# Kernel tuning notes

Hardware: AMD Instinct MI355X
Metric: run time of the kernel (lower is better)

Reference implementation:

```python
import jax, jax.numpy as jnp
import numpy as np

EPS = 0.05  # mesh.epsilon boundary band


def _pool_one(adj, image, vs, edges):
    # adj: [N,N] bool, image: [N,F] f32, vs: [N,2] f32 in [0,1], edges: [2,E] int32
    N, F = image.shape
    E = edges.shape[1]
    K = N // 2                      # out_target
    tgt_kills = N - K               # number of vertices removed
    v0, v1 = edges[0], edges[1]
    # heap key = sum of squares of concat(image[v0], image[v1])
    cost = jnp.sum(image[v0] * image[v0], -1) + jnp.sum(image[v1] * image[v1], -1)
    def bnd(p):
        return (p[:, 0] < EPS) | (p[:, 0] > 1 - EPS) | (p[:, 1] < EPS) | (p[:, 1] > 1 - EPS)
    ok = ~(bnd(vs[v0]) | bnd(vs[v1]))   # boundary_mask = ~is_boundary
    # heappop of [value, id] lists == stable sort by cost (ties broken by edge id)
    order = jnp.argsort(cost)
    # sequential greedy collapse: kill v1 if edge interior and both endpoints alive
    def step(carry, eid):
        mask, nk = carry
        a, b = v0[eid], v1[eid]
        acc = ok[eid] & mask[a] & mask[b] & (nk < tgt_kills)
        mask = mask.at[b].set(mask[b] & ~acc)
        return (mask, nk + acc.astype(jnp.int32)), acc
    (mask, _), accepts = jax.lax.scan(step, (jnp.ones(N, bool), jnp.int32(0)), order)
    sv0, sv1 = v0[order], v1[order]
    # mapping m: dead vertex -> absorbing vertex (identity elsewhere)
    dead = jnp.where(accepts, sv1, N)          # N = out-of-range -> dropped
    m = jnp.arange(N).at[dead].set(sv0, mode='drop')
    # update_matrix: scatter-add collapsed vertex features into absorber rows
    upd = jnp.zeros_like(image).at[jnp.where(accepts, sv0, N)].add(image[sv1], mode='drop')
    image2 = image + upd
    # merge_vertex on adjacency: union rows then columns of merged vertices
    A = adj.astype(jnp.uint8)
    A1 = jnp.zeros_like(A).at[m].max(A)        # merge rows
    A2 = jnp.zeros_like(A1).at[m].max(A1.T).T  # merge cols
    alive = jnp.nonzero(mask, size=K, fill_value=0)[0]  # exactly K survivors
    adj_out = A2[alive][:, alive].astype(bool) & ~jnp.eye(K, dtype=bool)
    return adj_out, image2[alive]


def setup_inputs() -> dict:
    key = jax.random.key(0)
    k1, k2, k3, k4, k5 = jax.random.split(key, 5)
    B, N, F, E = 4, 8192, 64, 65536
    adj = jax.random.bernoulli(k1, 0.002, (B, N, N))
    image = jax.random.normal(k2, (B, N, F), jnp.float32)
    vs = jax.random.uniform(k3, (B, N, 2), dtype=jnp.float32)
    a = jax.random.randint(k4, (B, 1, E), 0, N)
    off = jax.random.randint(k5, (B, 1, E), 1, N)
    b = (a + off) % N                           # guarantee v0 != v1
    edges = jnp.concatenate([a, b], axis=1).astype(jnp.int32)
    return {"adj": adj, "image": image, "vs": vs, "edges": edges}


def reference(adj, image, vs, edges):
    # returns (pooled adjacency [B,N//2,N//2] bool, pooled features [B,N//2,F])
    return jax.vmap(_pool_one)(adj, image, vs, edges)
```

## Files before the change

kernel.cpp:

```cpp
#include <hip/hip_runtime.h>
#include <stdint.h>

typedef unsigned long long u64;
typedef unsigned int u32;
typedef unsigned char u8;

#define Bn 4
#define Nv 8192
#define Fd 64
#define Ed 65536
#define Kv 4096
#define TGTK 4096
#define NW 256
#define SC 8192

#define SWZ8(i) ((i) ^ (((i) >> 3) & 15))

#define WS_FLAGS   ((size_t)0)
#define WS_ACCCNT  ((size_t)256)
#define WS_OUTBITS ((size_t)512)
#define OUTBITS_BYTES ((size_t)Bn*Kv*128*4)
#define WS_ZERO_BYTES (WS_OUTBITS + OUTBITS_BYTES)
#define WS_KEYS    (WS_ZERO_BYTES)
#define WS_SQ      (WS_KEYS + (size_t)Bn*Ed*8)
#define WS_BND     (WS_SQ + (size_t)Bn*Nv*4)
#define WS_MAP     (WS_BND + (size_t)Bn*Nv)
#define WS_POS     (WS_MAP + (size_t)Bn*Nv*4)
#define WS_PM      (WS_POS + (size_t)Bn*Nv*4)
#define WS_ALIVEW  (WS_PM + (size_t)Bn*Nv*4)
#define WS_ALIST   (WS_ALIVEW + (size_t)Bn*NW*4)
#define WS_ACC     (WS_ALIST + (size_t)Bn*Kv*4)
#define WS_PACK    (WS_ACC + (size_t)Bn*TGTK*2*4)
#define WS_SPACK   (WS_PACK + (size_t)Bn*Ed*4)

__global__ void k_detect(const u8* adj, u32* flags) {
    int tid = blockIdx.x * blockDim.x + threadIdx.x;
    const u32* w = (const u32*)adj;
    bool f0 = false, f1 = false, f2 = false, f3 = false;
    for (int i = tid; i < (1 << 19); i += gridDim.x * blockDim.x) {
        u32 v = w[i];
        f0 |= (v & 0x000000FFu) != 0;
        f1 |= (v & 0x0000FF00u) != 0;
        f2 |= (v & 0x00FF0000u) != 0;
        f3 |= (v & 0xFF000000u) != 0;
    }
    u32 m = 0;
    if (__ballot(f0)) m |= 1;
    if (__ballot(f1)) m |= 2;
    if (__ballot(f2)) m |= 4;
    if (__ballot(f3)) m |= 8;
    if ((threadIdx.x & 63) == 0 && m) atomicOr(flags, m);
}

__global__ void k_vertex(const float* image, const float* vs, float* sq, u8* bnd, int* map) {
#pragma clang fp contract(off)
    int idx = blockIdx.x * 256 + threadIdx.x;
    if (idx >= Bn * Nv) return;
    const float* row = image + (size_t)idx * Fd;
    float r[8];
#pragma unroll
    for (int j = 0; j < 8; ++j) r[j] = row[j] * row[j];
#pragma unroll
    for (int i = 8; i < 64; i += 8)
#pragma unroll
        for (int j = 0; j < 8; ++j) r[j] += row[i + j] * row[i + j];
    float s = ((r[0] + r[1]) + (r[2] + r[3])) + ((r[4] + r[5]) + (r[6] + r[7]));
    sq[idx] = s;
    float x = vs[(size_t)idx * 2], y = vs[(size_t)idx * 2 + 1];
    const float LO = 0.05f;
    const float HI = (float)(1.0 - 0.05);
    bnd[idx] = ((x < LO) || (x > HI) || (y < LO) || (y > HI)) ? 1 : 0;
    map[idx] = idx & (Nv - 1);
}

__global__ void k_edge(const int* edges, const float* sq, const u8* bnd, u64* keys, u32* pack) {
    int idx = blockIdx.x * 256 + threadIdx.x;
    if (idx >= Bn * Ed) return;
    int b = idx >> 16, e = idx & (Ed - 1);
    int v0 = edges[(size_t)b * 2 * Ed + e];
    int v1 = edges[(size_t)b * 2 * Ed + Ed + e];
    float c = sq[b * Nv + v0] + sq[b * Nv + v1];
    u32 okk = (!bnd[b * Nv + v0] && !bnd[b * Nv + v1]) ? 1u : 0u;
    pack[idx] = (u32)v0 | ((u32)v1 << 13) | (okk << 26);
    keys[idx] = okk ? (((u64)__float_as_uint(c) << 16) | (u32)e) : ~0ull;
}

__device__ __forceinline__ void bitonic_cas(u64* s, int i, int pa, bool asc) {
    u64 a = s[i], c = s[pa];
    if ((a > c) == asc) { s[i] = c; s[pa] = a; }
}
__device__ __forceinline__ void cex(u64& a, u64& b, bool asc) {
    if ((a > b) == asc) { u64 t = a; a = b; b = t; }
}

__global__ __launch_bounds__(1024) void k_sortA(u64* keys) {
    __shared__ u64 s[SC];
    int b = blockIdx.x >> 3, ch = blockIdx.x & 7;
    u64* base = keys + (size_t)b * Ed + (size_t)ch * SC;
    int gb = ch * SC;
    int t8 = threadIdx.x * 8;
    u64 r[8];
#pragma unroll
    for (int u = 0; u < 8; ++u) r[u] = base[t8 + u];
    cex(r[0], r[1], true); cex(r[2], r[3], false); cex(r[4], r[5], true); cex(r[6], r[7], false);
    cex(r[0], r[2], true); cex(r[1], r[3], true); cex(r[4], r[6], false); cex(r[5], r[7], false);
    cex(r[0], r[1], true); cex(r[2], r[3], true); cex(r[4], r[5], false); cex(r[6], r[7], false);
    {
        bool a8 = (((gb + t8) & 8) == 0);
        cex(r[0], r[4], a8); cex(r[1], r[5], a8); cex(r[2], r[6], a8); cex(r[3], r[7], a8);
        cex(r[0], r[2], a8); cex(r[1], r[3], a8); cex(r[4], r[6], a8); cex(r[5], r[7], a8);
        cex(r[0], r[1], a8); cex(r[2], r[3], a8); cex(r[4], r[5], a8); cex(r[6], r[7], a8);
    }
#pragma unroll
    for (int u = 0; u < 8; ++u) s[SWZ8(t8 + u)] = r[u];
    __syncthreads();
    for (int k = 16; k <= SC; k <<= 1) {
        for (int j = k >> 1; j >= 8; j >>= 1) {
#pragma unroll
            for (int p = 0; p < SC / 2048; ++p) {
                int t = p * 1024 + threadIdx.x;
                int i = ((t & ~(j - 1)) << 1) | (t & (j - 1));
                bool asc = (((gb + i) & k) == 0);
                bitonic_cas(s, SWZ8(i), SWZ8(i | j), asc);
            }
            __syncthreads();
        }
        bool asc = (((gb + t8) & k) == 0);
#pragma unroll
        for (int u = 0; u < 8; ++u) r[u] = s[SWZ8(t8 + u)];
        cex(r[0], r[4], asc); cex(r[1], r[5], asc); cex(r[2], r[6], asc); cex(r[3], r[7], asc);
        cex(r[0], r[2], asc); cex(r[1], r[3], asc); cex(r[4], r[6], asc); cex(r[5], r[7], asc);
        cex(r[0], r[1], asc); cex(r[2], r[3], asc); cex(r[4], r[5], asc); cex(r[6], r[7], asc);
        if (k == SC) {
#pragma unroll
            for (int u = 0; u < 8; ++u) base[t8 + u] = r[u];
        } else {
#pragma unroll
            for (int u = 0; u < 8; ++u) s[SWZ8(t8 + u)] = r[u];
            __syncthreads();
        }
    }
}

__global__ __launch_bounds__(1024) void k_sortV(u64* keys, int k) {
    int b = blockIdx.x >> 3;
    int c = (blockIdx.x & 7) * 1024 + threadIdx.x;
    u64* base = keys + (size_t)b * Ed + c;
    u64 r[8];
#pragma unroll
    for (int m = 0; m < 8; ++m) r[m] = base[(size_t)m * 8192];
    if (k == 65536) {
        cex(r[0], r[4], true); cex(r[1], r[5], true); cex(r[2], r[6], true); cex(r[3], r[7], true);
        cex(r[0], r[2], true); cex(r[1], r[3], true); cex(r[4], r[6], true); cex(r[5], r[7], true);
        cex(r[0], r[1], true); cex(r[2], r[3], true); cex(r[4], r[5], true); cex(r[6], r[7], true);
    } else if (k == 32768) {
        cex(r[0], r[2], true); cex(r[1], r[3], true); cex(r[4], r[6], false); cex(r[5], r[7], false);
        cex(r[0], r[1], true); cex(r[2], r[3], true); cex(r[4], r[5], false); cex(r[6], r[7], false);
    } else {
        cex(r[0], r[1], true); cex(r[2], r[3], false); cex(r[4], r[5], true); cex(r[6], r[7], false);
    }
#pragma unroll
    for (int m = 0; m < 8; ++m) base[(size_t)m * 8192] = r[m];
}

__global__ __launch_bounds__(1024) void k_sortC(u64* keys, int k,
                                                const u32* pack, u32* spack, int dofin) {
    __shared__ u64 s[SC];
    int b = blockIdx.x >> 3, ch = blockIdx.x & 7;
    u64* base = keys + (size_t)b * Ed + (size_t)ch * SC;
    int gb = ch * SC;
    for (int p = 0; p < SC / 1024; ++p) {
        int i = p * 1024 + threadIdx.x;
        s[SWZ8(i)] = base[i];
    }
    __syncthreads();
    bool asc = ((gb & k) == 0);
    for (int j = SC / 2; j >= 8; j >>= 1) {
#pragma unroll
        for (int p = 0; p < SC / 2048; ++p) {
            int t = p * 1024 + threadIdx.x;
            int i = ((t & ~(j - 1)) << 1) | (t & (j - 1));
            bitonic_cas(s, SWZ8(i), SWZ8(i | j), asc);
        }
        __syncthreads();
    }
    int t8 = threadIdx.x * 8;
    u64 r[8];
#pragma unroll
    for (int u = 0; u < 8; ++u) r[u] = s[SWZ8(t8 + u)];
    cex(r[0], r[4], asc); cex(r[1], r[5], asc); cex(r[2], r[6], asc); cex(r[3], r[7], asc);
    cex(r[0], r[2], asc); cex(r[1], r[3], asc); cex(r[4], r[6], asc); cex(r[5], r[7], asc);
    cex(r[0], r[1], asc); cex(r[2], r[3], asc); cex(r[4], r[5], asc); cex(r[6], r[7], asc);
    if (dofin) {
        const u32* pk = pack + (size_t)b * Ed;
        u32* sp = spack + (size_t)b * Ed + (size_t)ch * SC;
#pragma unroll
        for (int u = 0; u < 8; ++u)
            sp[t8 + u] = (r[u] == ~0ull) ? 0u : pk[(u32)(r[u] & 0xFFFFu)];
    } else {
#pragma unroll
        for (int u = 0; u < 8; ++u) base[t8 + u] = r[u];
    }
}

__global__ __launch_bounds__(64) void k_greedy(const u32* spack, int* map, u32* aliveW,
                                               int* accList, u32* accCnt) {
    int b = blockIdx.x;
    int lane = threadIdx.x;
    __shared__ u32 alive[NW];
    __shared__ u32 mlane[Nv];
    for (int i = lane; i < NW; i += 64) alive[i] = 0xFFFFFFFFu;
    for (int i = lane; i < Nv; i += 64) mlane[i] = 0x7FFFFFFFu;
    const u32* sp = spack + (size_t)b * Ed;
    u32 pa = sp[lane], pb = sp[64 + lane];
    __syncthreads();
    int nk = 0;
    const int G = Ed / 128;
    for (int g = 0; g < G; ++g) {
        u32 na = 0u, nb = 0u;
        if (g + 1 < G) { na = sp[(g + 1) * 128 + lane]; nb = sp[(g + 1) * 128 + 64 + lane]; }
        int v0a = pa & 8191, v1a = (pa >> 13) & 8191; bool oka = (pa >> 26) & 1u;
        int v0b = pb & 8191, v1b = (pb >> 13) & 8191; bool okb = (pb >> 26) & 1u;
        u32 gi = (u32)(G + 1 - g) << 8;
        if (oka) atomicMin(&mlane[v1a], gi | (u32)lane);
        if (okb) atomicMin(&mlane[v1b], gi | (u32)(64 + lane));
        __syncthreads();
        u32 aw0a = alive[v0a >> 5], aw1a = alive[v1a >> 5];
        u32 aw0b = alive[v0b >> 5], aw1b = alive[v1b >> 5];
        u32 m0a = mlane[v0a], m1a = mlane[v1a];
        u32 m0b = mlane[v0b], m1b = mlane[v1b];
        bool specA = oka && ((aw0a >> (v0a & 31)) & 1u) && ((aw1a >> (v1a & 31)) & 1u);
        bool specB = okb && ((aw0b >> (v0b & 31)) & 1u) && ((aw1b >> (v1b & 31)) & 1u);
        u32 slA = (u32)lane, slB = (u32)(64 + lane);
        bool confA = specA && ((((m0a & 0xFFFFFF00u) == gi) && ((m0a & 255u) < slA)) ||
                               (((m1a & 0xFFFFFF00u) == gi) && ((m1a & 255u) < slA)));
        bool confB = specB && ((((m0b & 0xFFFFFF00u) == gi) && ((m0b & 255u) < slB)) ||
                               (((m1b & 0xFFFFFF00u) == gi) && ((m1b & 255u) < slB)));
        u64 specLo = __ballot(specA), specHi = __ballot(specB);
        u64 confLo = __ballot(confA), confHi = __ballot(confB);
        u64 accLo = specLo & ~confLo, accHi = specHi & ~confHi;
        u64 rem = confLo;
        while (rem) {
            int l = __ffsll((unsigned long long)rem) - 1; rem &= rem - 1;
            int bv0 = __shfl(v0a, l), bv1 = __shfl(v1a, l);
            bool kA = ((accLo >> lane) & 1ull) && (lane < l) && (v1a == bv0 || v1a == bv1);
            if (__ballot(kA) == 0ull) accLo |= 1ull << l;
        }
        rem = confHi;
        while (rem) {
            int l = __ffsll((unsigned long long)rem) - 1; rem &= rem - 1;
            int bv0 = __shfl(v0b, l), bv1 = __shfl(v1b, l);
            bool kA = ((accLo >> lane) & 1ull) && (v1a == bv0 || v1a == bv1);
            bool kB = ((accHi >> lane) & 1ull) && (lane < l) && (v1b == bv0 || v1b == bv1);
            if ((__ballot(kA) | __ballot(kB)) == 0ull) accHi |= 1ull << l;
        }
        int cntLo = __popcll(accLo);
        int cnt = cntLo + __popcll(accHi);
        int remK = TGTK - nk;
        bool accA = (accLo >> lane) & 1ull;
        bool accB = (accHi >> lane) & 1ull;
        if (cnt > remK) {
            int rA = __popcll(accLo & ((1ull << lane) - 1ull));
            if (accA && rA >= remK) accA = false;
            int rB = cntLo + __popcll(accHi & ((1ull << lane) - 1ull));
            if (accB && rB >= remK) accB = false;
            accLo = __ballot(accA); accHi = __ballot(accB);
            cntLo = __popcll(accLo);
            cnt = remK;
        }
        if (accA) {
            atomicAnd(&alive[v1a >> 5], ~(1u << (v1a & 31)));
            map[(size_t)b * Nv + v1a] = v0a;
            int r = __popcll(accLo & ((1ull << lane) - 1ull));
            int slot = nk + r;
            accList[((size_t)b * TGTK + slot) * 2] = v0a;
            accList[((size_t)b * TGTK + slot) * 2 + 1] = v1a;
        }
        if (accB) {
            atomicAnd(&alive[v1b >> 5], ~(1u << (v1b & 31)));
            map[(size_t)b * Nv + v1b] = v0b;
            int r = cntLo + __popcll(accHi & ((1ull << lane) - 1ull));
            int slot = nk + r;
            accList[((size_t)b * TGTK + slot) * 2] = v0b;
            accList[((size_t)b * TGTK + slot) * 2 + 1] = v1b;
        }
        nk += cnt;
        if (nk >= TGTK) break;
        pa = na; pb = nb;
    }
    for (int i = lane; i < NW; i += 64) aliveW[b * NW + i] = alive[i];
    if (lane == 0) accCnt[b] = (u32)nk;
}

__global__ __launch_bounds__(256) void k_scan(const u32* aliveW, const int* map,
                                              int* pos, int* pm, int* alist) {
    int b = blockIdx.x, tid = threadIdx.x;
    __shared__ u32 cnt[256];
    __shared__ u32 off[256];
    u32 w = aliveW[b * NW + tid];
    cnt[tid] = __popc(w);
    __syncthreads();
    if (tid == 0) { u32 s = 0; for (int i = 0; i < 256; ++i) { off[i] = s; s += cnt[i]; } }
    __syncthreads();
    u32 base = off[tid];
    int* posb = pos + (size_t)b * Nv;
    int* alb = alist + (size_t)b * Kv;
    for (int bit = 0; bit < 32; ++bit) {
        int v = tid * 32 + bit;
        int p = -1;
        if ((w >> bit) & 1u) {
            if (base < Kv) { p = (int)base; alb[base] = v; }
            base++;
        }
        posb[v] = p;
    }
    __syncthreads();
    const int* mapb = map + (size_t)b * Nv;
    int* pmb = pm + (size_t)b * Nv;
    for (int v = tid; v < Nv; v += 256) pmb[v] = posb[mapb[v]];
}

__global__ void k_fcopy(const float* image, const int* alist, float* outF) {
    int idx = blockIdx.x * 256 + threadIdx.x;
    if (idx >= Bn * Kv * 16) return;
    int b = idx >> 16, r = idx & 65535;
    int x = r >> 4, f4 = r & 15;
    int src = alist[b * Kv + x];
    const float4* s = (const float4*)(image + ((size_t)(b * Nv + src)) * Fd) + f4;
    float4* d = (float4*)(outF + ((size_t)(b * Kv + x)) * Fd) + f4;
    *d = *s;
}

__global__ __launch_bounds__(64) void k_fscat(const float* image, const int* accList,
                                              const u32* accCnt, const int* pos, float* outF) {
    int b = blockIdx.x >> 12, e = blockIdx.x & 4095;
    if (e >= (int)accCnt[b]) return;
    int v0 = accList[((size_t)b * TGTK + e) * 2];
    int v1 = accList[((size_t)b * TGTK + e) * 2 + 1];
    int x = pos[(size_t)b * Nv + v0];
    if (x < 0) return;
    int f = threadIdx.x;
    atomicAdd(outF + ((size_t)(b * Kv + x)) * Fd + f,
              image[((size_t)(b * Nv + v1)) * Fd + f]);
}

__global__ __launch_bounds__(256) void k_merge(const u8* adj, const u32* flags,
                                               const int* pm, u32* outbits) {
    int bi = blockIdx.x;
    int b = bi >> 13, i = bi & (Nv - 1);
    int t = pm[(size_t)b * Nv + i];
    if (t < 0) return;
    __shared__ u32 bits[Kv / 32];
    int tid = threadIdx.x;
    if (tid < 128) bits[tid] = 0;
    __syncthreads();
    const int* pmb = pm + (size_t)b * Nv;
    u32 fw = flags[0];
    bool bytefmt = (fw & 1) && (fw & 8);
    auto put = [&](int col) {
        int c = pmb[col];
        if (c >= 0) atomicOr(&bits[c >> 5], 1u << (c & 31));
    };
    if (bytefmt) {
        const uint4* row = (const uint4*)(adj + ((size_t)b * Nv + i) * Nv);
#pragma unroll
        for (int it = 0; it < 2; ++it) {
            uint4 v = row[it * 256 + tid];
            if (v.x | v.y | v.z | v.w) {
                int cb = (it * 256 + tid) * 16;
                u32 wv[4] = { v.x, v.y, v.z, v.w };
                for (int q = 0; q < 4; ++q) {
                    u32 u = wv[q];
                    if (!u) continue;
#pragma unroll
                    for (int kk = 0; kk < 4; ++kk)
                        if ((u >> (8 * kk)) & 0xFFu) put(cb + q * 4 + kk);
                }
            }
        }
    } else {
        const uint4* row = (const uint4*)((const u32*)adj + ((size_t)b * Nv + i) * Nv);
        for (int it = 0; it < 8; ++it) {
            uint4 v = row[it * 256 + tid];
            int cb = (it * 256 + tid) * 4;
            if (v.x) put(cb);
            if (v.y) put(cb + 1);
            if (v.z) put(cb + 2);
            if (v.w) put(cb + 3);
        }
    }
    __syncthreads();
    if (tid < 128) {
        u32 bw = bits[tid];
        if (bw) atomicOr(&outbits[((size_t)b * Kv + t) * 128 + tid], bw);
    }
}

__global__ void k_expand(const u32* outbits, float* out) {
    int idx = blockIdx.x;
    int tid = threadIdx.x;
    int b = idx >> 14, r = idx & 16383;
    int x = r >> 2, seg = r & 3;
    int c0 = seg * 1024 + tid * 4;
    u32 w = outbits[((size_t)b * Kv + x) * 128 + (c0 >> 5)];
    u32 nib = (w >> (c0 & 31)) & 0xFu;
    float4 f;
    f.x = (nib & 1) ? 1.f : 0.f;
    f.y = (nib & 2) ? 1.f : 0.f;
    f.z = (nib & 4) ? 1.f : 0.f;
    f.w = (nib & 8) ? 1.f : 0.f;
    if (x >= c0 && x < c0 + 4) ((float*)&f)[x - c0] = 0.f;
    *((float4*)(out + ((size_t)(b * Kv + x)) * Kv + c0)) = f;
}

extern "C" void kernel_launch(void* const* d_in, const int* in_sizes, int n_in,
                              void* d_out, int out_size, void* d_ws, size_t ws_size,
                              hipStream_t stream) {
    const u8* adj = (const u8*)d_in[0];
    const float* image = (const float*)d_in[1];
    const float* vs = (const float*)d_in[2];
    const int* edges = (const int*)d_in[3];
    char* ws = (char*)d_ws;
    u32* flags = (u32*)(ws + WS_FLAGS);
    u32* accCnt = (u32*)(ws + WS_ACCCNT);
    u32* outbits = (u32*)(ws + WS_OUTBITS);
    u64* keys = (u64*)(ws + WS_KEYS);
    float* sq = (float*)(ws + WS_SQ);
    u8* bnd = (u8*)(ws + WS_BND);
    int* map = (int*)(ws + WS_MAP);
    int* pos = (int*)(ws + WS_POS);
    int* pm = (int*)(ws + WS_PM);
    u32* aliveW = (u32*)(ws + WS_ALIVEW);
    int* alist = (int*)(ws + WS_ALIST);
    int* accList = (int*)(ws + WS_ACC);
    u32* pack = (u32*)(ws + WS_PACK);
    u32* spack = (u32*)(ws + WS_SPACK);
    float* outA = (float*)d_out;
    float* outF = outA + (size_t)Bn * Kv * Kv;

    hipMemsetAsync(d_ws, 0, WS_ZERO_BYTES, stream);
    k_detect<<<64, 256, 0, stream>>>(adj, flags);
    k_vertex<<<Bn * Nv / 256, 256, 0, stream>>>(image, vs, sq, bnd, map);
    k_edge<<<Bn * Ed / 256, 256, 0, stream>>>(edges, sq, bnd, keys, pack);
    k_sortA<<<Bn * 8, 1024, 0, stream>>>(keys);
    k_sortV<<<Bn * 8, 1024, 0, stream>>>(keys, 16384);
    k_sortC<<<Bn * 8, 1024, 0, stream>>>(keys, 16384, pack, spack, 0);
    k_sortV<<<Bn * 8, 1024, 0, stream>>>(keys, 32768);
    k_sortC<<<Bn * 8, 1024, 0, stream>>>(keys, 32768, pack, spack, 0);
    k_sortV<<<Bn * 8, 1024, 0, stream>>>(keys, 65536);
    k_sortC<<<Bn * 8, 1024, 0, stream>>>(keys, 65536, pack, spack, 1);
    k_greedy<<<Bn, 64, 0, stream>>>(spack, map, aliveW, accList, accCnt);
    k_scan<<<Bn, 256, 0, stream>>>(aliveW, map, pos, pm, alist);
    k_fcopy<<<Bn * Kv * 16 / 256, 256, 0, stream>>>(image, alist, outF);
    k_fscat<<<Bn * TGTK, 64, 0, stream>>>(image, accList, accCnt, pos, outF);
    k_merge<<<Bn * Nv, 256, 0, stream>>>(adj, flags, pm, outbits);
    k_expand<<<Bn * Kv * 4, 256, 0, stream>>>(outbits, outA);
}
```

Before: 1.761 ms.

## Fuse detect into vertex, sort V+C stages, and scan into greedy kernel

Folds the adjacency-format detection into the first 64 blocks of the vertex kernel, and merges each global bitonic cross-chunk step with the following in-shared-memory chunk sort so each block recomputes the needed cross-chunk compare-exchanges while loading. The alive-bitmap prefix scan and position mapping move into the tail of the single-wave greedy kernel, using shuffles and shared memory instead of a separate launch. This removes five kernel launches and a global round trip of the key array per merge stage. In exchange, the fused sort kernel reads 2-8x more key data per block, and the scan now runs on only 64 threads per batch.

```diff
diff --git a/kernel.cpp b/kernel.cpp
--- a/kernel.cpp
+++ b/kernel.cpp
@@ -27,34 +27,32 @@
 #define WS_MAP     (WS_BND + (size_t)Bn*Nv)
 #define WS_POS     (WS_MAP + (size_t)Bn*Nv*4)
 #define WS_PM      (WS_POS + (size_t)Bn*Nv*4)
-#define WS_ALIVEW  (WS_PM + (size_t)Bn*Nv*4)
-#define WS_ALIST   (WS_ALIVEW + (size_t)Bn*NW*4)
+#define WS_ALIST   (WS_PM + (size_t)Bn*Nv*4)
 #define WS_ACC     (WS_ALIST + (size_t)Bn*Kv*4)
 #define WS_PACK    (WS_ACC + (size_t)Bn*TGTK*2*4)
 #define WS_SPACK   (WS_PACK + (size_t)Bn*Ed*4)
 
-__global__ void k_detect(const u8* adj, u32* flags) {
-    int tid = blockIdx.x * blockDim.x + threadIdx.x;
-    const u32* w = (const u32*)adj;
-    bool f0 = false, f1 = false, f2 = false, f3 = false;
-    for (int i = tid; i < (1 << 19); i += gridDim.x * blockDim.x) {
-        u32 v = w[i];
-        f0 |= (v & 0x000000FFu) != 0;
-        f1 |= (v & 0x0000FF00u) != 0;
-        f2 |= (v & 0x00FF0000u) != 0;
-        f3 |= (v & 0xFF000000u) != 0;
-    }
-    u32 m = 0;
-    if (__ballot(f0)) m |= 1;
-    if (__ballot(f1)) m |= 2;
-    if (__ballot(f2)) m |= 4;
-    if (__ballot(f3)) m |= 8;
-    if ((threadIdx.x & 63) == 0 && m) atomicOr(flags, m);
-}
-
-__global__ void k_vertex(const float* image, const float* vs, float* sq, u8* bnd, int* map) {
+__global__ void k_vertex(const float* image, const float* vs, float* sq, u8* bnd, int* map,
+                         const u8* adj, u32* flags) {
 #pragma clang fp contract(off)
     int idx = blockIdx.x * 256 + threadIdx.x;
+    if (blockIdx.x < 64) {
+        const u32* w = (const u32*)adj;
+        bool f0 = false, f1 = false, f2 = false, f3 = false;
+        for (int i = idx; i < (1 << 19); i += 16384) {
+            u32 v = w[i];
+            f0 |= (v & 0x000000FFu) != 0;
+            f1 |= (v & 0x0000FF00u) != 0;
+            f2 |= (v & 0x00FF0000u) != 0;
+            f3 |= (v & 0xFF000000u) != 0;
+        }
+        u32 m = 0;
+        if (__ballot(f0)) m |= 1;
+        if (__ballot(f1)) m |= 2;
+        if (__ballot(f2)) m |= 4;
+        if (__ballot(f3)) m |= 8;
+        if ((threadIdx.x & 63) == 0 && m) atomicOr(flags, m);
+    }
     if (idx >= Bn * Nv) return;
     const float* row = image + (size_t)idx * Fd;
     float r[8];
@@ -142,36 +140,45 @@
     }
 }
 
-__global__ __launch_bounds__(1024) void k_sortV(u64* keys, int k) {
-    int b = blockIdx.x >> 3;
-    int c = (blockIdx.x & 7) * 1024 + threadIdx.x;
-    u64* base = keys + (size_t)b * Ed + c;
-    u64 r[8];
-#pragma unroll
-    for (int m = 0; m < 8; ++m) r[m] = base[(size_t)m * 8192];
-    if (k == 65536) {
-        cex(r[0], r[4], true); cex(r[1], r[5], true); cex(r[2], r[6], true); cex(r[3], r[7], true);
-        cex(r[0], r[2], true); cex(r[1], r[3], true); cex(r[4], r[6], true); cex(r[5], r[7], true);
-        cex(r[0], r[1], true); cex(r[2], r[3], true); cex(r[4], r[5], true); cex(r[6], r[7], true);
-    } else if (k == 32768) {
-        cex(r[0], r[2], true); cex(r[1], r[3], true); cex(r[4], r[6], false); cex(r[5], r[7], false);
-        cex(r[0], r[1], true); cex(r[2], r[3], true); cex(r[4], r[5], false); cex(r[6], r[7], false);
-    } else {
-        cex(r[0], r[1], true); cex(r[2], r[3], false); cex(r[4], r[5], true); cex(r[6], r[7], false);
-    }
-#pragma unroll
-    for (int m = 0; m < 8; ++m) base[(size_t)m * 8192] = r[m];
-}
-
-__global__ __launch_bounds__(1024) void k_sortC(u64* keys, int k,
-                                                const u32* pack, u32* spack, int dofin) {
+__global__ __launch_bounds__(1024) void k_sortVC(u64* keys, int k,
+                                                 const u32* pack, u32* spack, int dofin) {
     __shared__ u64 s[SC];
     int b = blockIdx.x >> 3, ch = blockIdx.x & 7;
-    u64* base = keys + (size_t)b * Ed + (size_t)ch * SC;
+    const size_t bofs = (size_t)b * Ed;
     int gb = ch * SC;
-    for (int p = 0; p < SC / 1024; ++p) {
-        int i = p * 1024 + threadIdx.x;
-        s[SWZ8(i)] = base[i];
+    if (k == 65536) {
+        for (int p = 0; p < 8; ++p) {
+            int c = p * 1024 + threadIdx.x;
+            u64 v[8];
+#pragma unroll
+            for (int m = 0; m < 8; ++m) v[m] = keys[bofs + (size_t)m * SC + c];
+            cex(v[0], v[4], true); cex(v[1], v[5], true); cex(v[2], v[6], true); cex(v[3], v[7], true);
+            cex(v[0], v[2], true); cex(v[1], v[3], true); cex(v[4], v[6], true); cex(v[5], v[7], true);
+            cex(v[0], v[1], true); cex(v[2], v[3], true); cex(v[4], v[5], true); cex(v[6], v[7], true);
+            s[SWZ8(c)] = v[ch];
+        }
+    } else if (k == 32768) {
+        int g4 = ch & 4;
+        bool adir = (ch < 4);
+        for (int p = 0; p < 8; ++p) {
+            int c = p * 1024 + threadIdx.x;
+            u64 v[4];
+#pragma unroll
+            for (int m = 0; m < 4; ++m) v[m] = keys[bofs + (size_t)(g4 + m) * SC + c];
+            cex(v[0], v[2], adir); cex(v[1], v[3], adir);
+            cex(v[0], v[1], adir); cex(v[2], v[3], adir);
+            s[SWZ8(c)] = v[ch & 3];
+        }
+    } else {
+        int g2 = ch & 6;
+        bool adir = ((ch & 2) == 0);
+        for (int p = 0; p < 8; ++p) {
+            int c = p * 1024 + threadIdx.x;
+            u64 v0 = keys[bofs + (size_t)g2 * SC + c];
+            u64 v1 = keys[bofs + (size_t)(g2 + 1) * SC + c];
+            cex(v0, v1, adir);
+            s[SWZ8(c)] = (ch & 1) ? v1 : v0;
+        }
     }
     __syncthreads();
     bool asc = ((gb & k) == 0);
@@ -192,19 +199,21 @@
     cex(r[0], r[2], asc); cex(r[1], r[3], asc); cex(r[4], r[6], asc); cex(r[5], r[7], asc);
     cex(r[0], r[1], asc); cex(r[2], r[3], asc); cex(r[4], r[5], asc); cex(r[6], r[7], asc);
     if (dofin) {
-        const u32* pk = pack + (size_t)b * Ed;
-        u32* sp = spack + (size_t)b * Ed + (size_t)ch * SC;
+        const u32* pk = pack + bofs;
+        u32* sp = spack + bofs + (size_t)ch * SC;
 #pragma unroll
         for (int u = 0; u < 8; ++u)
             sp[t8 + u] = (r[u] == ~0ull) ? 0u : pk[(u32)(r[u] & 0xFFFFu)];
     } else {
+        u64* base = keys + bofs + (size_t)ch * SC;
 #pragma unroll
         for (int u = 0; u < 8; ++u) base[t8 + u] = r[u];
     }
 }
 
-__global__ __launch_bounds__(64) void k_greedy(const u32* spack, int* map, u32* aliveW,
-                                               int* accList, u32* accCnt) {
+__global__ __launch_bounds__(64) void k_greedy(const u32* spack, int* map,
+                                               int* accList, u32* accCnt,
+                                               int* pos, int* pm, int* alist) {
     int b = blockIdx.x;
     int lane = threadIdx.x;
     __shared__ u32 alive[NW];
@@ -288,36 +297,39 @@
         if (nk >= TGTK) break;
         pa = na; pb = nb;
     }
-    for (int i = lane; i < NW; i += 64) aliveW[b * NW + i] = alive[i];
     if (lane == 0) accCnt[b] = (u32)nk;
-}
-
-__global__ __launch_bounds__(256) void k_scan(const u32* aliveW, const int* map,
-                                              int* pos, int* pm, int* alist) {
-    int b = blockIdx.x, tid = threadIdx.x;
-    __shared__ u32 cnt[256];
-    __shared__ u32 off[256];
-    u32 w = aliveW[b * NW + tid];
-    cnt[tid] = __popc(w);
-    __syncthreads();
-    if (tid == 0) { u32 s = 0; for (int i = 0; i < 256; ++i) { off[i] = s; s += cnt[i]; } }
-    __syncthreads();
-    u32 base = off[tid];
+    __syncthreads();
+    __threadfence();
+    u32 w0 = alive[lane * 4], w1 = alive[lane * 4 + 1];
+    u32 w2 = alive[lane * 4 + 2], w3 = alive[lane * 4 + 3];
+    u32 c0 = __popc(w0), c1 = __popc(w1), c2 = __popc(w2), c3 = __popc(w3);
+    u32 lsum = c0 + c1 + c2 + c3;
+    u32 incl = lsum;
+#pragma unroll
+    for (int d = 1; d < 64; d <<= 1) { u32 t = __shfl_up(incl, d); if (lane >= d) incl += t; }
+    u32 base = incl - lsum;
     int* posb = pos + (size_t)b * Nv;
     int* alb = alist + (size_t)b * Kv;
-    for (int bit = 0; bit < 32; ++bit) {
-        int v = tid * 32 + bit;
-        int p = -1;
-        if ((w >> bit) & 1u) {
-            if (base < Kv) { p = (int)base; alb[base] = v; }
-            base++;
-        }
-        posb[v] = p;
+    __syncthreads();
+    u32 wv[4] = { w0, w1, w2, w3 };
+    for (int q = 0; q < 4; ++q) {
+        u32 w = wv[q];
+        int vb = lane * 128 + q * 32;
+        for (int bit = 0; bit < 32; ++bit) {
+            int v = vb + bit;
+            int p = -1;
+            if ((w >> bit) & 1u) {
+                if (base < Kv) { p = (int)base; alb[base] = v; }
+                base++;
+            }
+            mlane[v] = (u32)p;
+            posb[v] = p;
+        }
     }
     __syncthreads();
     const int* mapb = map + (size_t)b * Nv;
     int* pmb = pm + (size_t)b * Nv;
-    for (int v = tid; v < Nv; v += 256) pmb[v] = posb[mapb[v]];
+    for (int v = lane; v < Nv; v += 64) pmb[v] = (int)mlane[(u32)mapb[v]];
 }
 
 __global__ void k_fcopy(const float* image, const int* alist, float* outF) {
@@ -430,7 +442,6 @@
     int* map = (int*)(ws + WS_MAP);
     int* pos = (int*)(ws + WS_POS);
     int* pm = (int*)(ws + WS_PM);
-    u32* aliveW = (u32*)(ws + WS_ALIVEW);
     int* alist = (int*)(ws + WS_ALIST);
     int* accList = (int*)(ws + WS_ACC);
     u32* pack = (u32*)(ws + WS_PACK);
@@ -439,18 +450,13 @@
     float* outF = outA + (size_t)Bn * Kv * Kv;
 
     hipMemsetAsync(d_ws, 0, WS_ZERO_BYTES, stream);
-    k_detect<<<64, 256, 0, stream>>>(adj, flags);
-    k_vertex<<<Bn * Nv / 256, 256, 0, stream>>>(image, vs, sq, bnd, map);
+    k_vertex<<<Bn * Nv / 256, 256, 0, stream>>>(image, vs, sq, bnd, map, adj, flags);
     k_edge<<<Bn * Ed / 256, 256, 0, stream>>>(edges, sq, bnd, keys, pack);
     k_sortA<<<Bn * 8, 1024, 0, stream>>>(keys);
-    k_sortV<<<Bn * 8, 1024, 0, stream>>>(keys, 16384);
-    k_sortC<<<Bn * 8, 1024, 0, stream>>>(keys, 16384, pack, spack, 0);
-    k_sortV<<<Bn * 8, 1024, 0, stream>>>(keys, 32768);
-    k_sortC<<<Bn * 8, 1024, 0, stream>>>(keys, 32768, pack, spack, 0);
-    k_sortV<<<Bn * 8, 1024, 0, stream>>>(keys, 65536);
-    k_sortC<<<Bn * 8, 1024, 0, stream>>>(keys, 65536, pack, spack, 1);
-    k_greedy<<<Bn, 64, 0, stream>>>(spack, map, aliveW, accList, accCnt);
-    k_scan<<<Bn, 256, 0, stream>>>(aliveW, map, pos, pm, alist);
+    k_sortVC<<<Bn * 8, 1024, 0, stream>>>(keys, 16384, pack, spack, 0);
+    k_sortVC<<<Bn * 8, 1024, 0, stream>>>(keys, 32768, pack, spack, 0);
+    k_sortVC<<<Bn * 8, 1024, 0, stream>>>(keys, 65536, pack, spack, 1);
+    k_greedy<<<Bn, 64, 0, stream>>>(spack, map, accList, accCnt, pos, pm, alist);
     k_fcopy<<<Bn * Kv * 16 / 256, 256, 0, stream>>>(image, alist, outF);
     k_fscat<<<Bn * TGTK, 64, 0, stream>>>(image, accList, accCnt, pos, outF);
     k_merge<<<Bn * Nv, 256, 0, stream>>>(adj, flags, pm, outbits);
```

New measurement: 1.788 ms. No clear change (+1.5%).

## Fuse detect, scan and outbits zeroing into neighboring kernels; widen expand blocks

Applied to the files above, without the earlier changes.

Folds the adjacency byte-layout detection into the vertex kernel and folds the alive-bit prefix scan and position mapping into the tail of the greedy kernel. The scan uses a wave shuffle and the shared mlane table for the pm lookup. Zeroing of the outbits buffer moves from the memset into the feature-copy kernel, so the memset shrinks to the flags. k_expand now processes a full output row per block, staging its bits in shared memory. The goal is fewer launches and less memset traffic, at the cost of serial scan work inside a 64-lane single-block-per-batch kernel.

```diff
diff --git a/kernel.cpp b/kernel.cpp
--- a/kernel.cpp
+++ b/kernel.cpp
@@ -18,43 +18,41 @@
 
 #define WS_FLAGS   ((size_t)0)
 #define WS_ACCCNT  ((size_t)256)
+#define WS_ZERO_BYTES ((size_t)512)
 #define WS_OUTBITS ((size_t)512)
 #define OUTBITS_BYTES ((size_t)Bn*Kv*128*4)
-#define WS_ZERO_BYTES (WS_OUTBITS + OUTBITS_BYTES)
-#define WS_KEYS    (WS_ZERO_BYTES)
+#define WS_KEYS    (WS_OUTBITS + OUTBITS_BYTES)
 #define WS_SQ      (WS_KEYS + (size_t)Bn*Ed*8)
 #define WS_BND     (WS_SQ + (size_t)Bn*Nv*4)
 #define WS_MAP     (WS_BND + (size_t)Bn*Nv)
 #define WS_POS     (WS_MAP + (size_t)Bn*Nv*4)
 #define WS_PM      (WS_POS + (size_t)Bn*Nv*4)
-#define WS_ALIVEW  (WS_PM + (size_t)Bn*Nv*4)
-#define WS_ALIST   (WS_ALIVEW + (size_t)Bn*NW*4)
+#define WS_ALIST   (WS_PM + (size_t)Bn*Nv*4)
 #define WS_ACC     (WS_ALIST + (size_t)Bn*Kv*4)
 #define WS_PACK    (WS_ACC + (size_t)Bn*TGTK*2*4)
 #define WS_SPACK   (WS_PACK + (size_t)Bn*Ed*4)
 
-__global__ void k_detect(const u8* adj, u32* flags) {
-    int tid = blockIdx.x * blockDim.x + threadIdx.x;
-    const u32* w = (const u32*)adj;
-    bool f0 = false, f1 = false, f2 = false, f3 = false;
-    for (int i = tid; i < (1 << 19); i += gridDim.x * blockDim.x) {
-        u32 v = w[i];
-        f0 |= (v & 0x000000FFu) != 0;
-        f1 |= (v & 0x0000FF00u) != 0;
-        f2 |= (v & 0x00FF0000u) != 0;
-        f3 |= (v & 0xFF000000u) != 0;
-    }
-    u32 m = 0;
-    if (__ballot(f0)) m |= 1;
-    if (__ballot(f1)) m |= 2;
-    if (__ballot(f2)) m |= 4;
-    if (__ballot(f3)) m |= 8;
-    if ((threadIdx.x & 63) == 0 && m) atomicOr(flags, m);
-}
-
-__global__ void k_vertex(const float* image, const float* vs, float* sq, u8* bnd, int* map) {
+__global__ void k_vertex(const float* image, const float* vs, float* sq, u8* bnd, int* map,
+                         const u8* adj, u32* flags) {
 #pragma clang fp contract(off)
     int idx = blockIdx.x * 256 + threadIdx.x;
+    if (blockIdx.x < 64) {
+        const u32* w = (const u32*)adj;
+        bool f0 = false, f1 = false, f2 = false, f3 = false;
+        for (int i = idx; i < (1 << 19); i += 16384) {
+            u32 v = w[i];
+            f0 |= (v & 0x000000FFu) != 0;
+            f1 |= (v & 0x0000FF00u) != 0;
+            f2 |= (v & 0x00FF0000u) != 0;
+            f3 |= (v & 0xFF000000u) != 0;
+        }
+        u32 m = 0;
+        if (__ballot(f0)) m |= 1;
+        if (__ballot(f1)) m |= 2;
+        if (__ballot(f2)) m |= 4;
+        if (__ballot(f3)) m |= 8;
+        if ((threadIdx.x & 63) == 0 && m) atomicOr(flags, m);
+    }
     if (idx >= Bn * Nv) return;
     const float* row = image + (size_t)idx * Fd;
     float r[8];
@@ -203,8 +201,9 @@
     }
 }
 
-__global__ __launch_bounds__(64) void k_greedy(const u32* spack, int* map, u32* aliveW,
-                                               int* accList, u32* accCnt) {
+__global__ __launch_bounds__(64) void k_greedy(const u32* spack, int* map,
+                                               int* accList, u32* accCnt,
+                                               int* pos, int* pm, int* alist) {
     int b = blockIdx.x;
     int lane = threadIdx.x;
     __shared__ u32 alive[NW];
@@ -288,41 +287,49 @@
         if (nk >= TGTK) break;
         pa = na; pb = nb;
     }
-    for (int i = lane; i < NW; i += 64) aliveW[b * NW + i] = alive[i];
     if (lane == 0) accCnt[b] = (u32)nk;
-}
-
-__global__ __launch_bounds__(256) void k_scan(const u32* aliveW, const int* map,
-                                              int* pos, int* pm, int* alist) {
-    int b = blockIdx.x, tid = threadIdx.x;
-    __shared__ u32 cnt[256];
-    __shared__ u32 off[256];
-    u32 w = aliveW[b * NW + tid];
-    cnt[tid] = __popc(w);
-    __syncthreads();
-    if (tid == 0) { u32 s = 0; for (int i = 0; i < 256; ++i) { off[i] = s; s += cnt[i]; } }
-    __syncthreads();
-    u32 base = off[tid];
+    __syncthreads();
+    __threadfence();
+    u32 w0 = alive[lane * 4], w1 = alive[lane * 4 + 1];
+    u32 w2 = alive[lane * 4 + 2], w3 = alive[lane * 4 + 3];
+    u32 c0 = __popc(w0), c1 = __popc(w1), c2 = __popc(w2), c3 = __popc(w3);
+    u32 lsum = c0 + c1 + c2 + c3;
+    u32 incl = lsum;
+#pragma unroll
+    for (int d = 1; d < 64; d <<= 1) { u32 t = __shfl_up(incl, d); if (lane >= d) incl += t; }
+    u32 base = incl - lsum;
     int* posb = pos + (size_t)b * Nv;
     int* alb = alist + (size_t)b * Kv;
-    for (int bit = 0; bit < 32; ++bit) {
-        int v = tid * 32 + bit;
-        int p = -1;
-        if ((w >> bit) & 1u) {
-            if (base < Kv) { p = (int)base; alb[base] = v; }
-            base++;
-        }
-        posb[v] = p;
+    __syncthreads();
+    u32 wv[4] = { w0, w1, w2, w3 };
+    for (int q = 0; q < 4; ++q) {
+        u32 w = wv[q];
+        int vb = lane * 128 + q * 32;
+        for (int bit = 0; bit < 32; ++bit) {
+            int v = vb + bit;
+            int p = -1;
+            if ((w >> bit) & 1u) {
+                if (base < Kv) { p = (int)base; alb[base] = v; }
+                base++;
+            }
+            mlane[v] = (u32)p;
+            posb[v] = p;
+        }
     }
     __syncthreads();
     const int* mapb = map + (size_t)b * Nv;
     int* pmb = pm + (size_t)b * Nv;
-    for (int v = tid; v < Nv; v += 256) pmb[v] = posb[mapb[v]];
-}
-
-__global__ void k_fcopy(const float* image, const int* alist, float* outF) {
+    for (int v = lane; v < Nv; v += 64) pmb[v] = (int)mlane[(u32)mapb[v]];
+}
+
+__global__ void k_fcopy(const float* image, const int* alist, float* outF, u32* outbits) {
     int idx = blockIdx.x * 256 + threadIdx.x;
     if (idx >= Bn * Kv * 16) return;
+    {
+        uint4* ob = (uint4*)(outbits + (size_t)idx * 8);
+        uint4 z = { 0, 0, 0, 0 };
+        ob[0] = z; ob[1] = z;
+    }
     int b = idx >> 16, r = idx & 65535;
     int x = r >> 4, f4 = r & 15;
     int src = alist[b * Kv + x];
@@ -396,21 +403,27 @@
     }
 }
 
-__global__ void k_expand(const u32* outbits, float* out) {
-    int idx = blockIdx.x;
+__global__ __launch_bounds__(256) void k_expand(const u32* outbits, float* out) {
+    int bi = blockIdx.x;
+    int b = bi >> 12, x = bi & (Kv - 1);
     int tid = threadIdx.x;
-    int b = idx >> 14, r = idx & 16383;
-    int x = r >> 2, seg = r & 3;
-    int c0 = seg * 1024 + tid * 4;
-    u32 w = outbits[((size_t)b * Kv + x) * 128 + (c0 >> 5)];
-    u32 nib = (w >> (c0 & 31)) & 0xFu;
-    float4 f;
-    f.x = (nib & 1) ? 1.f : 0.f;
-    f.y = (nib & 2) ? 1.f : 0.f;
-    f.z = (nib & 4) ? 1.f : 0.f;
-    f.w = (nib & 8) ? 1.f : 0.f;
-    if (x >= c0 && x < c0 + 4) ((float*)&f)[x - c0] = 0.f;
-    *((float4*)(out + ((size_t)(b * Kv + x)) * Kv + c0)) = f;
+    __shared__ u32 bits[128];
+    if (tid < 128) bits[tid] = outbits[((size_t)b * Kv + x) * 128 + tid];
+    __syncthreads();
+    float* rowOut = out + ((size_t)(b * Kv + x)) * Kv;
+#pragma unroll
+    for (int q = 0; q < 4; ++q) {
+        int c0 = q * 1024 + tid * 4;
+        u32 w = bits[c0 >> 5];
+        u32 nib = (w >> (c0 & 31)) & 0xFu;
+        float4 f;
+        f.x = (nib & 1) ? 1.f : 0.f;
+        f.y = (nib & 2) ? 1.f : 0.f;
+        f.z = (nib & 4) ? 1.f : 0.f;
+        f.w = (nib & 8) ? 1.f : 0.f;
+        if (x >= c0 && x < c0 + 4) ((float*)&f)[x - c0] = 0.f;
+        *((float4*)(rowOut + c0)) = f;
+    }
 }
 
 extern "C" void kernel_launch(void* const* d_in, const int* in_sizes, int n_in,
@@ -430,7 +443,6 @@
     int* map = (int*)(ws + WS_MAP);
     int* pos = (int*)(ws + WS_POS);
     int* pm = (int*)(ws + WS_PM);
-    u32* aliveW = (u32*)(ws + WS_ALIVEW);
     int* alist = (int*)(ws + WS_ALIST);
     int* accList = (int*)(ws + WS_ACC);
     u32* pack = (u32*)(ws + WS_PACK);
@@ -439,8 +451,7 @@
     float* outF = outA + (size_t)Bn * Kv * Kv;
 
     hipMemsetAsync(d_ws, 0, WS_ZERO_BYTES, stream);
-    k_detect<<<64, 256, 0, stream>>>(adj, flags);
-    k_vertex<<<Bn * Nv / 256, 256, 0, stream>>>(image, vs, sq, bnd, map);
+    k_vertex<<<Bn * Nv / 256, 256, 0, stream>>>(image, vs, sq, bnd, map, adj, flags);
     k_edge<<<Bn * Ed / 256, 256, 0, stream>>>(edges, sq, bnd, keys, pack);
     k_sortA<<<Bn * 8, 1024, 0, stream>>>(keys);
     k_sortV<<<Bn * 8, 1024, 0, stream>>>(keys, 16384);
@@ -449,10 +460,9 @@
     k_sortC<<<Bn * 8, 1024, 0, stream>>>(keys, 32768, pack, spack, 0);
     k_sortV<<<Bn * 8, 1024, 0, stream>>>(keys, 65536);
     k_sortC<<<Bn * 8, 1024, 0, stream>>>(keys, 65536, pack, spack, 1);
-    k_greedy<<<Bn, 64, 0, stream>>>(spack, map, aliveW, accList, accCnt);
-    k_scan<<<Bn, 256, 0, stream>>>(aliveW, map, pos, pm, alist);
-    k_fcopy<<<Bn * Kv * 16 / 256, 256, 0, stream>>>(image, alist, outF);
+    k_greedy<<<Bn, 64, 0, stream>>>(spack, map, accList, accCnt, pos, pm, alist);
+    k_fcopy<<<Bn * Kv * 16 / 256, 256, 0, stream>>>(image, alist, outF, outbits);
     k_fscat<<<Bn * TGTK, 64, 0, stream>>>(image, accList, accCnt, pos, outF);
     k_merge<<<Bn * Nv, 256, 0, stream>>>(adj, flags, pm, outbits);
-    k_expand<<<Bn * Kv * 4, 256, 0, stream>>>(outbits, outA);
-}
+    k_expand<<<Bn * Kv, 256, 0, stream>>>(outbits, outA);
+}
```

After: 1.760 ms. About the same (-0.1%).
